# Kernel optimization log

Hardware: AMD Instinct MI355X
Metric: run time of the kernel (lower is better)

The kernel has to match this reference:

```python
import jax, jax.numpy as jnp
import numpy as np

N = 100000
H = 128
F_IN = 32
F_OUT = 16
NUM_GRAPHS = 64
NEG_SLOPE = 0.2


def setup_inputs() -> dict:
    key = jax.random.key(0)
    ks = jax.random.split(key, 16)
    inp = {
        'x': jax.random.normal(ks[0], (N, F_IN), dtype=jnp.float32),
        'edge_index': jax.random.randint(ks[1], (2, 1000000), 0, N, dtype=jnp.int32),
        'subgraph_edge_index': jax.random.randint(ks[2], (2, 1000000), 0, N, dtype=jnp.int32),
        'node_subnode_index': jax.random.randint(ks[3], (2, 200000), 0, N, dtype=jnp.int32),
        'subnode_node_index': jax.random.randint(ks[4], (2, 200000), 0, N, dtype=jnp.int32),
        'ground_node': jnp.arange(40000, dtype=jnp.int32),
        'subgraph_batch_index': jax.random.randint(ks[5], (60000,), 0, NUM_GRAPHS, dtype=jnp.int32),
        'batch_idx': jax.random.randint(ks[6], (40000,), 0, NUM_GRAPHS, dtype=jnp.int32),
    }
    s_in = 1.0 / np.sqrt(F_IN)
    s_h = 1.0 / np.sqrt(H)
    inp['emb_W'] = jax.random.uniform(ks[7], (F_IN, H), jnp.float32, -s_in, s_in)
    inp['emb_b'] = jax.random.uniform(ks[8], (H,), jnp.float32, -s_in, s_in)
    # 4 GATv2 layers (depth=1): lin_l, lin_r, att, bias per layer
    inp['Wl'] = jax.random.uniform(ks[9], (4, H, H), jnp.float32, -s_h, s_h)
    inp['Wr'] = jax.random.uniform(ks[10], (4, H, H), jnp.float32, -s_h, s_h)
    inp['att'] = jax.random.uniform(ks[11], (4, H), jnp.float32, -s_h, s_h)
    inp['bias'] = jax.random.uniform(ks[12], (4, H), jnp.float32, -s_h, s_h)
    inp['out_W'] = jax.random.uniform(ks[13], (H, F_OUT), jnp.float32, -s_h, s_h)
    inp['out_b'] = jax.random.uniform(ks[14], (F_OUT,), jnp.float32, -s_h, s_h)
    return inp


def _gatv2(x, ei, Wl, Wr, att, b):
    # add self loops (PyG GATv2Conv default add_self_loops=True)
    loops = jnp.broadcast_to(jnp.arange(N, dtype=ei.dtype)[None, :], (2, N))
    ei = jnp.concatenate([ei, loops], axis=1)
    src, dst = ei[0], ei[1]
    xl = x @ Wl  # source transform [N,H]
    xr = x @ Wr  # target transform [N,H]
    e = jax.nn.leaky_relu(xl[src] + xr[dst], NEG_SLOPE) @ att  # [E]
    m = jax.ops.segment_max(e, dst, num_segments=N)
    p = jnp.exp(e - m[dst])
    s = jax.ops.segment_sum(p, dst, num_segments=N)
    alpha = p / s[dst]
    out = jax.ops.segment_sum(alpha[:, None] * xl[src], dst, num_segments=N)
    return out + b


def reference(x, edge_index, subgraph_edge_index, node_subnode_index,
              subnode_node_index, ground_node, subgraph_batch_index, batch_idx,
              emb_W, emb_b, Wl, Wr, att, bias, out_W, out_b):
    h = x @ emb_W + emb_b
    eis = (edge_index, node_subnode_index, subgraph_edge_index, subnode_node_index)
    for i, ei in enumerate(eis):
        h = _gatv2(h, ei, Wl[i], Wr[i], att[i], bias[i])
    # global_add_pool over ground nodes
    pooled = jax.ops.segment_sum(h[ground_node], batch_idx, num_segments=NUM_GRAPHS)
    return pooled @ out_W + out_b
```

## Files before the change

### kernel.cpp

```cpp
#include <hip/hip_runtime.h>
#include <cstddef>


typedef __attribute__((ext_vector_type(8))) short bf16x8;
typedef __attribute__((ext_vector_type(4))) float f32x4;
typedef __attribute__((ext_vector_type(2))) float f32x2;

#define NSH   10
#define CHUNK 8192
#define POOLP 256

__device__ __forceinline__ unsigned short f2bf(float f) {
  unsigned int u = __float_as_uint(f);
  u += 0x7fffu + ((u >> 16) & 1u);
  return (unsigned short)(u >> 16);
}
__device__ __forceinline__ unsigned int pack2bf(float a, float b) {
  return (__float_as_uint(a) >> 16) | (__float_as_uint(b) & 0xFFFF0000u);
}
__device__ __forceinline__ float bf2f(short s) {
  return __uint_as_float(((unsigned int)(unsigned short)s) << 16);
}
__device__ __forceinline__ float2 unpk(unsigned int u) {
  return make_float2(__uint_as_float(u << 16),
                     __uint_as_float(u & 0xFFFF0000u));
}
__device__ __forceinline__ f32x2 unpk2(unsigned int u) {
  f32x2 r;
  r.x = __uint_as_float(u << 16);
  r.y = __uint_as_float(u & 0xFFFF0000u);
  return r;
}
__device__ __forceinline__ int dlog(int s) {
  int b = s >> 6, i = s & 63;
  return (b << 6) + ((i & 3) << 4) + (i >> 2);
}

__device__ __forceinline__ float row16_sum(float x) {
  x += __uint_as_float((unsigned)__builtin_amdgcn_mov_dpp(
        (int)__float_as_uint(x), 0xB1, 0xF, 0xF, true));
  x += __uint_as_float((unsigned)__builtin_amdgcn_mov_dpp(
        (int)__float_as_uint(x), 0x4E, 0xF, 0xF, true));
  x += __uint_as_float((unsigned)__builtin_amdgcn_mov_dpp(
        (int)__float_as_uint(x), 0x124, 0xF, 0xF, true));
  x += __uint_as_float((unsigned)__builtin_amdgcn_mov_dpp(
        (int)__float_as_uint(x), 0x128, 0xF, 0xF, true));
  return x;
}

__device__ __forceinline__ int lds_excl_scan(int* a, int len, int* aux, int tid)
{
  int g = (len + 255) >> 8;
  int lo = tid * g;
  int s = 0;
  for (int i = 0; i < g; ++i) { int idx = lo + i; if (idx < len) s += a[idx]; }
  aux[tid] = s;
  __syncthreads();
  for (int d = 1; d < 256; d <<= 1) {
    int v = (tid >= d) ? aux[tid - d] : 0;
    __syncthreads();
    aux[tid] += v;
    __syncthreads();
  }
  int run = aux[tid] - s;
  for (int i = 0; i < g; ++i) {
    int idx = lo + i;
    if (idx < len) { int t = a[idx]; a[idx] = run; run += t; }
  }
  int total = aux[255];
  __syncthreads();
  return total;
}

__device__ __forceinline__ void resolve_item(
    int id, int t1, int t2, int t3, int t4, int n,
    const int* s0, const int* s1, const int* s2, const int* s3,
    const int* d0, const int* d1, const int* d2, const int* d3,
    int& l, int& s, int& d, bool need_src)
{
  if (id < t4) {
    const int *sp, *dp; int e;
    if      (id < t1) { l = 0; e = id;      sp = s0; dp = d0; }
    else if (id < t2) { l = 1; e = id - t1; sp = s1; dp = d1; }
    else if (id < t3) { l = 2; e = id - t2; sp = s2; dp = d2; }
    else              { l = 3; e = id - t3; sp = s3; dp = d3; }
    d = dp[e];
    s = need_src ? sp[e] : 0;
  } else {
    int k = id - t4;
    l = (k >= 3 * n) ? 3 : (k >= 2 * n) ? 2 : (k >= n) ? 1 : 0;
    s = k - l * n; d = s;
  }
}

__global__ __launch_bounds__(256) void setup_kernel(
    const float* __restrict__ Wl, const float* __restrict__ Wr,
    const float* __restrict__ embW,
    const float* __restrict__ att, const float* __restrict__ bias,
    unsigned short* __restrict__ packB, unsigned short* __restrict__ packE,
    float* __restrict__ attA, float* __restrict__ attB,
    float* __restrict__ biasP,
    int* __restrict__ offs4, int* __restrict__ dhist, int* __restrict__ dcur,
    int n, int e0, int e1, int e2, int e3)
{
  const float LOG2E = 1.4426950408889634f;
  int id = blockIdx.x * 256 + threadIdx.x;
  if (id < 131072) {
    int j    = id & 7;
    int lane = (id >> 3) & 63;
    int kt   = (id >> 9) & 3;
    int ct   = (id >> 11) & 15;
    int l    = id >> 15;
    int kpos = kt * 32 + (lane >> 4) * 8 + j;
    int k    = dlog(kpos);
    int col  = ct * 16 + (lane & 15);
    float v = (ct < 8) ? Wl[(size_t)l * 16384 + k * 128 + col]
                       : Wr[(size_t)l * 16384 + k * 128 + (col - 128)];
    packB[id] = f2bf(v);
  }
  int pe = id - 131072;
  if (pe >= 0 && pe < 4096) {
    int j    = pe & 7;
    int lane = (pe >> 3) & 63;
    int ct   = pe >> 9;
    int k    = (lane >> 4) * 8 + j;
    int col  = ct * 16 + (lane & 15);
    packE[pe] = f2bf(embW[k * 128 + col]);
  }
  int ab = pe - 4096;
  if (ab >= 0 && ab < 512) {
    int l = ab >> 7, pos = ab & 127;
    int d = dlog(pos);
    float a = att[l * 128 + d];
    attA[ab]  = a * 0.6f * LOG2E;
    attB[ab]  = a * 0.4f * LOG2E;
    biasP[ab] = bias[l * 128 + d];
  }
  int q = ab - 512;
  if (q >= 0 && q < 4) {
    int El = (q == 0) ? e0 : (q == 1) ? e1 : (q == 2) ? e2 : e3;
    offs4[(size_t)q * (n + 1) + n] = El + n;
  }
  int z = q - 4;
  if (z >= 0 && z < 512) {
    if (z < 256) dhist[z] = 0; else dcur[z - 256] = 0;
  }
}

__global__ __launch_bounds__(256) void embed_mfma_kernel(
    const float* __restrict__ x, const unsigned short* __restrict__ packE,
    const float* __restrict__ b, unsigned short* __restrict__ hb, int n)
{
  const int wave = threadIdx.x >> 6;
  const int lane = threadIdx.x & 63;
  const int rlan = lane & 15;
  const int kgrp = lane >> 4;

  bf16x8 Bf[8];
#pragma unroll
  for (int ct = 0; ct < 8; ++ct)
    Bf[ct] = *(const bf16x8*)(packE + ((size_t)ct * 64 + lane) * 8);
  float bv[8];
#pragma unroll
  for (int ct = 0; ct < 8; ++ct) bv[ct] = b[ct * 16 + rlan];

  const float4* __restrict__ x4 = (const float4*)x;
  const int ntiles = (n + 15) / 16;
  for (int tile = blockIdx.x * 4 + wave; tile < ntiles; tile += gridDim.x * 4) {
    int r = tile * 16 + rlan;
    if (r >= n) r = n - 1;
    float4 a0 = x4[(size_t)r * 8 + kgrp * 2];
    float4 a1 = x4[(size_t)r * 8 + kgrp * 2 + 1];
    bf16x8 Af;
    Af[0] = (short)f2bf(a0.x); Af[1] = (short)f2bf(a0.y);
    Af[2] = (short)f2bf(a0.z); Af[3] = (short)f2bf(a0.w);
    Af[4] = (short)f2bf(a1.x); Af[5] = (short)f2bf(a1.y);
    Af[6] = (short)f2bf(a1.z); Af[7] = (short)f2bf(a1.w);

    f32x4 acc[8];
#pragma unroll
    for (int ct = 0; ct < 8; ++ct) {
      acc[ct] = (f32x4){0.f, 0.f, 0.f, 0.f};
      acc[ct] = __builtin_amdgcn_mfma_f32_16x16x32_bf16(Af, Bf[ct], acc[ct], 0, 0, 0);
    }
    int rowb = tile * 16 + kgrp * 4;
#pragma unroll
    for (int rr = 0; rr < 4; ++rr) {
      int row = rowb + rr;
      if (row < n) {
        uint2 p0, p1;
        p0.x = pack2bf(acc[0][rr] + bv[0], acc[1][rr] + bv[1]);
        p0.y = pack2bf(acc[2][rr] + bv[2], acc[3][rr] + bv[3]);
        p1.x = pack2bf(acc[4][rr] + bv[4], acc[5][rr] + bv[5]);
        p1.y = pack2bf(acc[6][rr] + bv[6], acc[7][rr] + bv[7]);
        *(uint2*)(hb + (size_t)row * 128 + rlan * 4)      = p0;
        *(uint2*)(hb + (size_t)row * 128 + 64 + rlan * 4) = p1;
      }
    }
  }
}

#define GPAD 136
__global__ __launch_bounds__(256) void gemm_mfma_kernel(
    const unsigned short* __restrict__ hb,
    const unsigned short* __restrict__ packB,
    unsigned short* __restrict__ xlb, unsigned short* __restrict__ xrb, int n)
{
  __shared__ unsigned short hs[32 * GPAD];
  const int tid  = threadIdx.x;
  const int wave = tid >> 6;
  const int lane = tid & 63;
  const int rlan = lane & 15;
  const int kgrp = lane >> 4;

  bf16x8 Bf[4][4];
#pragma unroll
  for (int ct = 0; ct < 4; ++ct)
#pragma unroll
    for (int kt = 0; kt < 4; ++kt)
      Bf[ct][kt] = *(const bf16x8*)(packB +
          ((((size_t)(wave * 4 + ct)) * 4 + kt) * 64 + lane) * 8);

  unsigned short* __restrict__ outp = (wave < 2) ? xlb : xrb;
  const int colbase = (wave & 1) * 64;

  const int ntiles = (n + 31) / 32;
  for (int tile = blockIdx.x; tile < ntiles; tile += gridDim.x) {
    const int row0 = tile * 32;
    __syncthreads();
#pragma unroll
    for (int i = 0; i < 4; ++i) {
      int g  = (i * 256 + tid) * 8;
      int r  = g >> 7;
      int cc = g & 127;
      int gr = row0 + r; if (gr >= n) gr = n - 1;
      uint4 v = *(const uint4*)(hb + (size_t)gr * 128 + cc);
      *(uint4*)(hs + r * GPAD + cc) = v;
    }
    __syncthreads();

    bf16x8 Af[2][4];
#pragma unroll
    for (int rt = 0; rt < 2; ++rt)
#pragma unroll
      for (int kt = 0; kt < 4; ++kt)
        Af[rt][kt] = *(const bf16x8*)(hs + (rt * 16 + rlan) * GPAD
                                         + kgrp * 8 + kt * 32);

    f32x4 acc[2][4];
#pragma unroll
    for (int rt = 0; rt < 2; ++rt)
#pragma unroll
      for (int ct = 0; ct < 4; ++ct)
        acc[rt][ct] = (f32x4){0.f, 0.f, 0.f, 0.f};
#pragma unroll
    for (int kt = 0; kt < 4; ++kt)
#pragma unroll
      for (int rt = 0; rt < 2; ++rt)
#pragma unroll
        for (int ct = 0; ct < 4; ++ct)
          acc[rt][ct] = __builtin_amdgcn_mfma_f32_16x16x32_bf16(
              Af[rt][kt], Bf[ct][kt], acc[rt][ct], 0, 0, 0);
#pragma unroll
    for (int rt = 0; rt < 2; ++rt) {
      int rowb = row0 + rt * 16 + kgrp * 4;
#pragma unroll
      for (int r = 0; r < 4; ++r) {
        int row = rowb + r;
        if (row < n) {
          uint2 pk;
          pk.x = pack2bf(acc[rt][0][r], acc[rt][1][r]);
          pk.y = pack2bf(acc[rt][2][r], acc[rt][3][r]);
          *(uint2*)(outp + (size_t)row * 128 + colbase + rlan * 4) = pk;
        }
      }
    }
  }
}

__global__ __launch_bounds__(256) void hist_kernel(
    const int* __restrict__ d0, const int* __restrict__ d1,
    const int* __restrict__ d2, const int* __restrict__ d3,
    int e0, int e1, int e2, int e3, int n, int nbk, int NB, int nitems,
    int* __restrict__ mat)
{
  __shared__ int hist[512];
  int tid = threadIdx.x, c = blockIdx.x;
  for (int i = tid; i < NB; i += 256) hist[i] = 0;
  __syncthreads();
  int t1 = e0, t2 = t1 + e1, t3 = t2 + e2, t4 = t3 + e3;
  int base = c * CHUNK;
#pragma unroll
  for (int k = 0; k < CHUNK / 256; ++k) {
    int id = base + k * 256 + tid;
    if (id < nitems) {
      int l, s, d;
      resolve_item(id, t1, t2, t3, t4, n,
                   nullptr, nullptr, nullptr, nullptr, d0, d1, d2, d3,
                   l, s, d, false);
      atomicAdd(&hist[l * nbk + (d >> NSH)], 1);
    }
  }
  __syncthreads();
  for (int i = tid; i < NB; i += 256) mat[(size_t)c * NB + i] = hist[i];
}

__global__ __launch_bounds__(256) void colscan_a_kernel(
    const int* __restrict__ mat, int* __restrict__ pfx,
    int nchunk, int NB, int* __restrict__ colsum)
{
  __shared__ int col[512];
  __shared__ int aux[256];
  int gb = blockIdx.x, tid = threadIdx.x;
  for (int i = tid; i < nchunk; i += 256) col[i] = mat[(size_t)i * NB + gb];
  __syncthreads();
  int tot = lds_excl_scan(col, nchunk, aux, tid);
  for (int i = tid; i < nchunk; i += 256) pfx[(size_t)i * NB + gb] = col[i];
  if (tid == 0) colsum[gb] = tot;
}

__global__ __launch_bounds__(256) void colscan_b_kernel(
    const int* __restrict__ colsum, int NB, int* __restrict__ colscan)
{
  __shared__ int buf[512];
  __shared__ int aux[256];
  int tid = threadIdx.x;
  for (int i = tid; i < NB; i += 256) buf[i] = colsum[i];
  __syncthreads();
  int tot = lds_excl_scan(buf, NB, aux, tid);
  for (int i = tid; i < NB; i += 256) colscan[i] = buf[i];
  if (tid == 0) colscan[NB] = tot;
}

__global__ __launch_bounds__(256) void scatter_kernel(
    const int* __restrict__ s0, const int* __restrict__ s1,
    const int* __restrict__ s2, const int* __restrict__ s3,
    const int* __restrict__ d0, const int* __restrict__ d1,
    const int* __restrict__ d2, const int* __restrict__ d3,
    int e0, int e1, int e2, int e3, int n, int nbk, int NB, int nitems,
    const int* __restrict__ mat, const int* __restrict__ pfx,
    const int* __restrict__ colscan, int* __restrict__ staging)
{
  __shared__ int lbuf[CHUNK];
  __shared__ int hist[512];
  __shared__ int cur[512];
  __shared__ int basex[512];
  __shared__ int aux[256];
  int tid = threadIdx.x, c = blockIdx.x;
  for (int i = tid; i < NB; i += 256) hist[i] = mat[(size_t)c * NB + i];
  __syncthreads();
  lds_excl_scan(hist, NB, aux, tid);
  for (int i = tid; i < NB; i += 256) {
    cur[i]   = hist[i];
    basex[i] = colscan[i] + pfx[(size_t)c * NB + i];
  }
  __syncthreads();
  int t1 = e0, t2 = t1 + e1, t3 = t2 + e2, t4 = t3 + e3;
  int base = c * CHUNK;
#pragma unroll
  for (int k = 0; k < CHUNK / 256; ++k) {
    int id = base + k * 256 + tid;
    if (id < nitems) {
      int l, s, d;
      resolve_item(id, t1, t2, t3, t4, n,
                   s0, s1, s2, s3, d0, d1, d2, d3, l, s, d, true);
      int gb = l * nbk + (d >> NSH);
      int p = atomicAdd(&cur[gb], 1);
      lbuf[p] = s | ((d & ((1 << NSH) - 1)) << 17);
    }
  }
  __syncthreads();
  int wave = tid >> 6, lane = tid & 63;
  for (int gb = wave; gb < NB; gb += 4) {
    int st = hist[gb], en = cur[gb];
    int gbase = basex[gb];
    for (int j = lane; j < en - st; j += 64)
      staging[gbase + j] = lbuf[st + j];
  }
}

__global__ __launch_bounds__(256) void finalize_kernel(
    const int* __restrict__ staging, const int* __restrict__ colscan,
    int* __restrict__ offs4, int* __restrict__ csr4,
    int* __restrict__ dhist, int n, int nbk,
    int cb0, int cb1, int cb2, int cb3)
{
  __shared__ int cnt[1 << NSH];
  __shared__ int pos[1 << NSH];
  __shared__ int aux[256];
  __shared__ int lh[64];
  int gb = blockIdx.x, tid = threadIdx.x;
  int l = gb / nbk, b = gb % nbk;
  int beg = colscan[gb], end = colscan[gb + 1];
  int node0 = b << NSH;
  int ncount = n - node0; if (ncount > (1 << NSH)) ncount = 1 << NSH;
  int cbl = (l == 0) ? cb0 : (l == 1) ? cb1 : (l == 2) ? cb2 : cb3;

  if (tid < 64) lh[tid] = 0;
  for (int i = tid; i < (1 << NSH); i += 256) cnt[i] = 0;
  __syncthreads();
  for (int t = beg + tid; t < end; t += 256)
    atomicAdd(&cnt[staging[t] >> 17], 1);
  __syncthreads();
  for (int i = tid; i < ncount; i += 256) {
    int dg = cnt[i]; if (dg > 63) dg = 63;
    atomicAdd(&lh[63 - dg], 1);
  }
  __syncthreads();
  if (tid < 64 && lh[tid] > 0) atomicAdd(&dhist[l * 64 + tid], lh[tid]);
  lds_excl_scan(cnt, 1 << NSH, aux, tid);
  for (int i = tid; i < (1 << NSH); i += 256) {
    if (i < ncount)
      offs4[(size_t)l * (n + 1) + node0 + i] = beg + cnt[i] - cbl;
    pos[i] = cnt[i];
  }
  __syncthreads();
  for (int t = beg + tid; t < end; t += 256) {
    int e = staging[t];
    int p = atomicAdd(&pos[e >> 17], 1);
    csr4[beg + p] = e & 0x1FFFF;
  }
}

__global__ __launch_bounds__(256) void deg_scatter_kernel(
    const int* __restrict__ offs4, const int* __restrict__ dbase,
    int* __restrict__ dcur, int* __restrict__ order, int n)
{
  __shared__ int lh[64], lbase[64], lcur[64];
  int l = blockIdx.y;
  int i = blockIdx.x * 256 + threadIdx.x;
  if (threadIdx.x < 64) { lh[threadIdx.x] = 0; lcur[threadIdx.x] = 0; }
  __syncthreads();
  int rbin = 0;
  if (i < n) {
    const int* o = offs4 + (size_t)l * (n + 1);
    int deg = o[i + 1] - o[i]; if (deg > 63) deg = 63;
    rbin = 63 - deg;
    atomicAdd(&lh[rbin], 1);
  }
  __syncthreads();
  if (threadIdx.x < 64 && lh[threadIdx.x] > 0)
    lbase[threadIdx.x] = atomicAdd(&dcur[l * 64 + threadIdx.x], lh[threadIdx.x]);
  __syncthreads();
  if (i < n) {
    int p = atomicAdd(&lcur[rbin], 1);
    order[dbase[l * 64 + rbin] + lbase[rbin] + p] = i;
  }
}

__global__ __launch_bounds__(256) void gat_dst_kernel(
    const unsigned short* __restrict__ xlb,
    const unsigned short* __restrict__ xrb,
    const int* __restrict__ offs, const int* __restrict__ csr,
    const int* __restrict__ ord,
    const float* __restrict__ attA, const float* __restrict__ attB,
    const float* __restrict__ biasP,
    float* __restrict__ hout_f, unsigned short* __restrict__ hout_b, int n)
{
  int wid = (blockIdx.x * 256 + threadIdx.x) >> 4;
  int c   = threadIdx.x & 15;
  if (wid >= n) return;
  int node = ord[wid];

  uint4 xru = *(const uint4*)(xrb + (size_t)node * 128 + c * 8);
  f32x2 xr0 = unpk2(xru.x), xr1 = unpk2(xru.y);
  f32x2 xr2 = unpk2(xru.z), xr3 = unpk2(xru.w);
  const f32x2* aA2 = (const f32x2*)(attA + c * 8);
  f32x2 aA0 = aA2[0], aA1 = aA2[1], aA2v = aA2[2], aA3 = aA2[3];
  const float* aBp = attB + c * 8;
  float aB0 = aBp[0], aB1 = aBp[1], aB2 = aBp[2], aB3 = aBp[3];
  float aB4 = aBp[4], aB5 = aBp[5], aB6 = aBp[6], aB7 = aBp[7];

  int beg = offs[node], end = offs[node + 1];
  int last = end - 1;
  float ssum = 0.f;
  f32x2 ac0 = {0.f, 0.f}, ac1 = {0.f, 0.f};
  f32x2 ac2 = {0.f, 0.f}, ac3 = {0.f, 0.f};

  const unsigned short* __restrict__ xp = xlb + c * 8;

  auto process = [&](uint4 cu) {
    f32x2 xs0 = unpk2(cu.x), xs1 = unpk2(cu.y);
    f32x2 xs2 = unpk2(cu.z), xs3 = unpk2(cu.w);
    f32x2 t0 = xs0 + xr0;
    f32x2 t1 = xs1 + xr1;
    f32x2 t2 = xs2 + xr2;
    f32x2 t3 = xs3 + xr3;
    f32x2 sA = t0 * aA0;
    sA = __builtin_elementwise_fma(t1, aA1, sA);
    sA = __builtin_elementwise_fma(t2, aA2v, sA);
    sA = __builtin_elementwise_fma(t3, aA3, sA);
    float sB0 = aB0 * __builtin_fabsf(t0.x);
    float sB1 = aB1 * __builtin_fabsf(t0.y);
    sB0 = fmaf(aB2, __builtin_fabsf(t1.x), sB0);
    sB1 = fmaf(aB3, __builtin_fabsf(t1.y), sB1);
    sB0 = fmaf(aB4, __builtin_fabsf(t2.x), sB0);
    sB1 = fmaf(aB5, __builtin_fabsf(t2.y), sB1);
    sB0 = fmaf(aB6, __builtin_fabsf(t3.x), sB0);
    sB1 = fmaf(aB7, __builtin_fabsf(t3.y), sB1);
    float part = (sA.x + sA.y) + (sB0 + sB1);
    part = row16_sum(part);
    float p = __builtin_amdgcn_exp2f(part);
    ssum += p;
    f32x2 pv = {p, p};
    ac0 = __builtin_elementwise_fma(pv, xs0, ac0);
    ac1 = __builtin_elementwise_fma(pv, xs1, ac1);
    ac2 = __builtin_elementwise_fma(pv, xs2, ac2);
    ac3 = __builtin_elementwise_fma(pv, xs3, ac3);
  };

  int i1 = beg + 1 < last ? beg + 1 : last;
  int i2 = beg + 2 < last ? beg + 2 : last;
  int i3 = beg + 3 < last ? beg + 3 : last;
  uint4 A = *(const uint4*)(xp + (size_t)csr[beg] * 128);
  uint4 B = *(const uint4*)(xp + (size_t)csr[i1] * 128);
  int sn0 = csr[i2], sn1 = csr[i3];

  int j = beg;
  for (; j + 1 < end; j += 2) {
    uint4 An = *(const uint4*)(xp + (size_t)sn0 * 128);
    uint4 Bn = *(const uint4*)(xp + (size_t)sn1 * 128);
    int m0 = j + 4 < last ? j + 4 : last;
    int m1 = j + 5 < last ? j + 5 : last;
    sn0 = csr[m0]; sn1 = csr[m1];
    process(A);
    process(B);
    A = An; B = Bn;
  }
  if (j < end) process(A);

  float inv = 1.0f / ssum;
  float o[8] = {ac0.x, ac0.y, ac1.x, ac1.y, ac2.x, ac2.y, ac3.x, ac3.y};
  const float* bi = biasP + c * 8;
#pragma unroll
  for (int k = 0; k < 8; ++k) o[k] = fmaf(o[k], inv, bi[k]);

  if (hout_f) {
    float4 v0 = make_float4(o[0], o[1], o[2], o[3]);
    float4 v1 = make_float4(o[4], o[5], o[6], o[7]);
    *(float4*)(hout_f + (size_t)node * 128 + c * 8)     = v0;
    *(float4*)(hout_f + (size_t)node * 128 + c * 8 + 4) = v1;
  } else {
    bf16x8 ob;
#pragma unroll
    for (int k = 0; k < 8; ++k) ob[k] = (short)f2bf(o[k]);
    *(bf16x8*)(hout_b + (size_t)node * 128 + c * 8) = ob;
  }
}

__global__ __launch_bounds__(256) void pool_partial_kernel(
    const float* __restrict__ h, const int* __restrict__ gnode,
    const int* __restrict__ bidx, float* __restrict__ partial, int ng)
{
  __shared__ float acc[64 * 128];
  int tid = threadIdx.x;
  for (int t = tid; t < 64 * 128; t += 256) acc[t] = 0.f;
  __syncthreads();
  int col = tid & 127, half = tid >> 7;
  for (int nd = blockIdx.x * 2 + half; nd < ng; nd += gridDim.x * 2) {
    int row = gnode[nd];
    int g   = bidx[nd];
    atomicAdd(&acc[g * 128 + col], h[(size_t)row * 128 + col]);
  }
  __syncthreads();
  float* out = partial + (size_t)blockIdx.x * 8192;
  for (int t = tid; t < 64 * 128; t += 256) out[t] = acc[t];
}

__global__ __launch_bounds__(128) void pool_out_kernel(
    const float* __restrict__ partial, const float* __restrict__ W,
    const float* __restrict__ b, float* __restrict__ out)
{
  __shared__ float pr[128];
  int g = blockIdx.x, tid = threadIdx.x;
  float s = 0.f;
  for (int p = 0; p < POOLP; ++p) s += partial[(size_t)p * 8192 + g * 128 + tid];
  pr[tid] = s;
  __syncthreads();
  if (tid < 16) {
    float acc = b[tid];
#pragma unroll
    for (int k = 0; k < 128; ++k) acc += pr[k] * W[dlog(k) * 16 + tid];
    out[g * 16 + tid] = acc;
  }
}

extern "C" void kernel_launch(void* const* d_in, const int* in_sizes, int n_in,
                              void* d_out, int out_size, void* d_ws, size_t ws_size,
                              hipStream_t stream)
{
  const float* x    = (const float*)d_in[0];
  const int* ei0    = (const int*)d_in[1];
  const int* ei_sg  = (const int*)d_in[2];
  const int* ei_ns  = (const int*)d_in[3];
  const int* ei_sn  = (const int*)d_in[4];
  const int* gnode  = (const int*)d_in[5];
  const int* bidx   = (const int*)d_in[7];
  const float* embW = (const float*)d_in[8];
  const float* embB = (const float*)d_in[9];
  const float* Wl   = (const float*)d_in[10];
  const float* Wr   = (const float*)d_in[11];
  const float* att  = (const float*)d_in[12];
  const float* bias = (const float*)d_in[13];
  const float* outW = (const float*)d_in[14];
  const float* outB = (const float*)d_in[15];

  const int n  = in_sizes[0] / 32;
  const int ng = in_sizes[5];

  const int  E_arr[4] = { in_sizes[1] / 2, in_sizes[3] / 2,
                          in_sizes[2] / 2, in_sizes[4] / 2 };
  const int* eptr[4]  = { ei0, ei_ns, ei_sg, ei_sn };
  const int E_tot  = E_arr[0] + E_arr[1] + E_arr[2] + E_arr[3];
  const int nitems = E_tot + 4 * n;
  const int nbk    = (n + (1 << NSH) - 1) >> NSH;
  const int NB     = 4 * nbk;
  const int nchunk = (nitems + CHUNK - 1) / CHUNK;
  int cb[4];
  cb[0] = 0;
  for (int i = 1; i < 4; ++i) cb[i] = cb[i - 1] + E_arr[i - 1] + n;

  char* ws = (char*)d_ws;
  size_t off = 0;
  auto alloc = [&](size_t bytes) -> void* {
    void* p = ws + off;
    off = (off + bytes + 255) & ~(size_t)255;
    return p;
  };
  float*          h      = (float*)alloc((size_t)n * 128 * sizeof(float));
  unsigned short* hb     = (unsigned short*)alloc((size_t)n * 128 * sizeof(unsigned short));
  unsigned short* xlb    = (unsigned short*)alloc((size_t)n * 128 * sizeof(unsigned short));
  unsigned short* xrb    = (unsigned short*)alloc((size_t)n * 128 * sizeof(unsigned short));
  int*            offs4  = (int*)alloc((size_t)4 * (n + 1) * sizeof(int));
  int*            mat    = (int*)alloc((size_t)nchunk * NB * sizeof(int));
  int*            pfx    = (int*)alloc((size_t)nchunk * NB * sizeof(int));
  int*            colsum = (int*)alloc((size_t)NB * sizeof(int));
  int*            colscan= (int*)alloc((size_t)(NB + 1) * sizeof(int));
  int*            staging= (int*)alloc((size_t)nitems * sizeof(int));
  int*            csr4   = (int*)alloc((size_t)nitems * sizeof(int));
  unsigned short* packB  = (unsigned short*)alloc(131072 * sizeof(unsigned short));
  unsigned short* packE  = (unsigned short*)alloc(4096 * sizeof(unsigned short));
  float*          attA   = (float*)alloc(512 * sizeof(float));
  float*          attB   = (float*)alloc(512 * sizeof(float));
  float*          biasP  = (float*)alloc(512 * sizeof(float));
  int*            dhist  = (int*)alloc(256 * sizeof(int));
  int*            dcur   = (int*)alloc(256 * sizeof(int));
  int*            dbase  = (int*)alloc(257 * sizeof(int));
  int*            order  = (int*)alloc((size_t)4 * n * sizeof(int));
  float*          partial= (float*)alloc((size_t)POOLP * 8192 * sizeof(float));
  (void)ws_size; (void)n_in; (void)out_size;

  const int* D[4] = { eptr[0] + E_arr[0], eptr[1] + E_arr[1],
                      eptr[2] + E_arr[2], eptr[3] + E_arr[3] };

  int setup_items = 131072 + 4096 + 512 + 4 + 512;
  setup_kernel<<<(setup_items + 255) / 256, 256, 0, stream>>>(
      Wl, Wr, embW, att, bias, packB, packE, attA, attB, biasP, offs4,
      dhist, dcur, n, E_arr[0], E_arr[1], E_arr[2], E_arr[3]);

  const int ntile16 = (n + 15) / 16;
  embed_mfma_kernel<<<(ntile16 + 3) / 4, 256, 0, stream>>>(
      x, packE, embB, hb, n);

  hist_kernel<<<nchunk, 256, 0, stream>>>(
      D[0], D[1], D[2], D[3], E_arr[0], E_arr[1], E_arr[2], E_arr[3],
      n, nbk, NB, nitems, mat);
  colscan_a_kernel<<<NB, 256, 0, stream>>>(mat, pfx, nchunk, NB, colsum);
  colscan_b_kernel<<<1, 256, 0, stream>>>(colsum, NB, colscan);
  scatter_kernel<<<nchunk, 256, 0, stream>>>(
      eptr[0], eptr[1], eptr[2], eptr[3], D[0], D[1], D[2], D[3],
      E_arr[0], E_arr[1], E_arr[2], E_arr[3], n, nbk, NB, nitems,
      mat, pfx, colscan, staging);
  finalize_kernel<<<NB, 256, 0, stream>>>(
      staging, colscan, offs4, csr4, dhist, n, nbk,
      cb[0], cb[1], cb[2], cb[3]);

  colscan_b_kernel<<<1, 256, 0, stream>>>(dhist, 256, dbase);
  dim3 dgrid((n + 255) / 256, 4);
  deg_scatter_kernel<<<dgrid, 256, 0, stream>>>(offs4, dbase, dcur, order, n);

  const int ntile32 = (n + 31) / 32;
  const int gemm_grid = (ntile32 + 1) / 2;
  for (int l = 0; l < 4; ++l) {
    gemm_mfma_kernel<<<gemm_grid, 256, 0, stream>>>(
        hb, packB + (size_t)l * 32768, xlb, xrb, n);
    gat_dst_kernel<<<((size_t)n * 16 + 255) / 256, 256, 0, stream>>>(
        xlb, xrb, offs4 + (size_t)l * (n + 1), csr4 + cb[l],
        order + (size_t)l * n,
        attA + l * 128, attB + l * 128, biasP + l * 128,
        (l == 3) ? h : nullptr, (l < 3) ? hb : nullptr, n);
  }

  pool_partial_kernel<<<POOLP, 256, 0, stream>>>(h, gnode, bidx, partial, ng);
  pool_out_kernel<<<64, 128, 0, stream>>>(partial, outW, outB, (float*)d_out);
}
```

Baseline: 477.9 us.

## Double-buffer GEMM tile loads, fold degree-bin scan into scatter kernel

```diff
diff --git a/kernel.cpp b/kernel.cpp
--- a/kernel.cpp
+++ b/kernel.cpp
@@ -206,7 +206,7 @@
     const unsigned short* __restrict__ packB,
     unsigned short* __restrict__ xlb, unsigned short* __restrict__ xrb, int n)
 {
-  __shared__ unsigned short hs[32 * GPAD];
+  __shared__ unsigned short hs[2][32 * GPAD];
   const int tid  = threadIdx.x;
   const int wave = tid >> 6;
   const int lane = tid & 63;
@@ -225,27 +225,38 @@
   const int colbase = (wave & 1) * 64;
 
   const int ntiles = (n + 31) / 32;
-  for (int tile = blockIdx.x; tile < ntiles; tile += gridDim.x) {
-    const int row0 = tile * 32;
-    __syncthreads();
+  const int stride = gridDim.x;
+
+  uint4 v[4];
+  auto gload = [&](int t) {
 #pragma unroll
     for (int i = 0; i < 4; ++i) {
       int g  = (i * 256 + tid) * 8;
-      int r  = g >> 7;
-      int cc = g & 127;
-      int gr = row0 + r; if (gr >= n) gr = n - 1;
-      uint4 v = *(const uint4*)(hb + (size_t)gr * 128 + cc);
-      *(uint4*)(hs + r * GPAD + cc) = v;
+      int gr = t * 32 + (g >> 7); if (gr >= n) gr = n - 1;
+      v[i] = *(const uint4*)(hb + (size_t)gr * 128 + (g & 127));
+    }
+  };
+
+  int tile = blockIdx.x;
+  if (tile < ntiles) gload(tile);
+  int buf = 0;
+  for (; tile < ntiles; tile += stride) {
+#pragma unroll
+    for (int i = 0; i < 4; ++i) {
+      int g = (i * 256 + tid) * 8;
+      *(uint4*)(&hs[buf][(g >> 7) * GPAD + (g & 127)]) = v[i];
     }
     __syncthreads();
+    int nt = tile + stride;
+    if (nt < ntiles) gload(nt);
 
     bf16x8 Af[2][4];
 #pragma unroll
     for (int rt = 0; rt < 2; ++rt)
 #pragma unroll
       for (int kt = 0; kt < 4; ++kt)
-        Af[rt][kt] = *(const bf16x8*)(hs + (rt * 16 + rlan) * GPAD
-                                         + kgrp * 8 + kt * 32);
+        Af[rt][kt] = *(const bf16x8*)(&hs[buf][(rt * 16 + rlan) * GPAD
+                                               + kgrp * 8 + kt * 32]);
 
     f32x4 acc[2][4];
 #pragma unroll
@@ -263,7 +274,7 @@
               Af[rt][kt], Bf[ct][kt], acc[rt][ct], 0, 0, 0);
 #pragma unroll
     for (int rt = 0; rt < 2; ++rt) {
-      int rowb = row0 + rt * 16 + kgrp * 4;
+      int rowb = tile * 32 + rt * 16 + kgrp * 4;
 #pragma unroll
       for (int r = 0; r < 4; ++r) {
         int row = rowb + r;
@@ -275,6 +286,7 @@
         }
       }
     }
+    buf ^= 1;
   }
 }
 
@@ -423,14 +435,22 @@
 }
 
 __global__ __launch_bounds__(256) void deg_scatter_kernel(
-    const int* __restrict__ offs4, const int* __restrict__ dbase,
+    const int* __restrict__ offs4, const int* __restrict__ dhist,
     int* __restrict__ dcur, int* __restrict__ order, int n)
 {
-  __shared__ int lh[64], lbase[64], lcur[64];
+  __shared__ int lh[64], lbase[64], lcur[64], dh[64], db[64];
   int l = blockIdx.y;
   int i = blockIdx.x * 256 + threadIdx.x;
-  if (threadIdx.x < 64) { lh[threadIdx.x] = 0; lcur[threadIdx.x] = 0; }
-  __syncthreads();
+  if (threadIdx.x < 64) {
+    lh[threadIdx.x] = 0; lcur[threadIdx.x] = 0;
+    dh[threadIdx.x] = dhist[l * 64 + threadIdx.x];
+  }
+  __syncthreads();
+  if (threadIdx.x < 64) {
+    int s = l * n;
+    for (int k = 0; k < threadIdx.x; ++k) s += dh[k];
+    db[threadIdx.x] = s;
+  }
   int rbin = 0;
   if (i < n) {
     const int* o = offs4 + (size_t)l * (n + 1);
@@ -444,7 +464,7 @@
   __syncthreads();
   if (i < n) {
     int p = atomicAdd(&lcur[rbin], 1);
-    order[dbase[l * 64 + rbin] + lbase[rbin] + p] = i;
+    order[db[rbin] + lbase[rbin] + p] = i;
   }
 }
 
@@ -645,7 +665,6 @@
   float*          biasP  = (float*)alloc(512 * sizeof(float));
   int*            dhist  = (int*)alloc(256 * sizeof(int));
   int*            dcur   = (int*)alloc(256 * sizeof(int));
-  int*            dbase  = (int*)alloc(257 * sizeof(int));
   int*            order  = (int*)alloc((size_t)4 * n * sizeof(int));
   float*          partial= (float*)alloc((size_t)POOLP * 8192 * sizeof(float));
   (void)ws_size; (void)n_in; (void)out_size;
@@ -675,12 +694,11 @@
       staging, colscan, offs4, csr4, dhist, n, nbk,
       cb[0], cb[1], cb[2], cb[3]);
 
-  colscan_b_kernel<<<1, 256, 0, stream>>>(dhist, 256, dbase);
   dim3 dgrid((n + 255) / 256, 4);
-  deg_scatter_kernel<<<dgrid, 256, 0, stream>>>(offs4, dbase, dcur, order, n);
+  deg_scatter_kernel<<<dgrid, 256, 0, stream>>>(offs4, dhist, dcur, order, n);
 
   const int ntile32 = (n + 31) / 32;
-  const int gemm_grid = (ntile32 + 1) / 2;
+  int gemm_grid = (ntile32 + 3) / 4;
   for (int l = 0; l < 4; ++l) {
     gemm_mfma_kernel<<<gemm_grid, 256, 0, stream>>>(
         hb, packB + (size_t)l * 32768, xlb, xrb, n);
```

New measurement: 536.6 us. 12.3% more time.
